# Kernel tuning notes

Hardware: AMD Instinct MI355X
Metric: run time of the kernel (lower is better)

Reference implementation:

```python
import jax, jax.numpy as jnp
import numpy as np

T, B, D, H, A = 512, 256, 256, 256, 8
LOG_STD_MIN, LOG_STD_MAX = -20.0, 2.0


def setup_inputs() -> dict:
    key = jax.random.key(0)
    ks = jax.random.split(key, 5)
    scaled = lambda k, sh, sc: (jax.random.normal(k, sh, jnp.float32) * sc)
    return {
        "x": jax.random.normal(ks[0], (T, B, D), jnp.float32),
        "carry0": jnp.zeros((B, H), jnp.float32),
        # GRU input kernels (ir|iz|in) packed: [D, 3H], shared input bias [3H]
        "Wi": scaled(ks[1], (D, 3 * H), 1.0 / np.sqrt(D)),
        "bi": jnp.zeros((3 * H,), jnp.float32),
        # GRU recurrent kernels (hr|hz|hn) packed: [H, 3H]; only hn has a bias
        "Wh": scaled(ks[2], (H, 3 * H), 1.0 / np.sqrt(H)),
        "bhn": jnp.zeros((H,), jnp.float32),
        # head Dense(2*A) with uniform(0.001)-style small init
        "Wo": scaled(ks[3], (H, 2 * A), 0.001),
        "bo": jnp.zeros((2 * A,), jnp.float32),
    }


def _gru_rollout(x, carry0, Wi, bi, Wh, bhn):
    h_dim = carry0.shape[-1]
    # Precompute input-side gate activations for all timesteps: [T, B, 3H]
    gates_x = x @ Wi + bi

    def step(h, gx):
        gh = h @ Wh  # [B, 3H]
        r = jax.nn.sigmoid(gx[..., :h_dim] + gh[..., :h_dim])
        z = jax.nn.sigmoid(gx[..., h_dim:2 * h_dim] + gh[..., h_dim:2 * h_dim])
        n = jnp.tanh(gx[..., 2 * h_dim:] + r * (gh[..., 2 * h_dim:] + bhn))
        h_new = (1.0 - z) * n + z * h
        return h_new, h_new

    _, carries = jax.lax.scan(step, carry0, gates_x)  # carries: [T, B, H]
    return carries


def reference(x, carry0, Wi, bi, Wh, bhn, Wo, bo):
    carries = _gru_rollout(x, carry0, Wi, bi, Wh, bhn)
    # head -> split into mean / log_std (StdType.MLP_HEAD), clip, exp
    y = carries @ Wo + bo  # [T, B, 2A]
    mean, log_std = jnp.split(y, 2, axis=-1)
    std = jnp.exp(jnp.clip(log_std, LOG_STD_MIN, LOG_STD_MAX))
    # distribution parameters of MultivariateNormalDiag, concatenated
    return jnp.concatenate([mean, std], axis=-1)  # [T, B, 2A]
```

## Files before the change

kernel.cpp:

```cpp
#include <hip/hip_runtime.h>
#include <hip/hip_fp16.h>

typedef _Float16 f16;
typedef __attribute__((ext_vector_type(8))) _Float16 f16x8;
typedef __attribute__((ext_vector_type(4))) _Float16 f16x4;
typedef __attribute__((ext_vector_type(4))) float f32x4;
typedef __attribute__((ext_vector_type(4))) float float4v;
typedef __attribute__((ext_vector_type(4))) int i32x4;

typedef __attribute__((address_space(3))) unsigned int lds_u32;
typedef const __attribute__((address_space(1))) unsigned int glb_u32;


#define CS 0.0039370079f
#define CHEAD 4.805919e-7f
#define FMAGIC 12582912.0f
#define IMAGIC 1262485504

static __device__ __forceinline__ float sigm_s(float x) {
  return __builtin_amdgcn_rcpf(1.0f + __expf(-0.0078125f * x));
}
static __device__ __forceinline__ float tanh_s(float x) {
  float e = __expf(0.015625f * x);
  return 1.0f - 2.0f * __builtin_amdgcn_rcpf(e + 1.0f);
}

__global__ void k_prep_wit(const float* __restrict__ Wi, f16* __restrict__ WiT) {
  __shared__ float tile[32][33];
  const int n0 = blockIdx.x * 32;
  const int k0 = blockIdx.y * 32;
  const int tx = threadIdx.x, ty = threadIdx.y;
#pragma unroll
  for (int i = 0; i < 4; ++i)
    tile[ty + i * 8][tx] = Wi[(size_t)(k0 + ty + i * 8) * 768 + n0 + tx];
  __syncthreads();
#pragma unroll
  for (int i = 0; i < 4; ++i)
    WiT[(size_t)(n0 + ty + i * 8) * 256 + k0 + tx] = (f16)tile[tx][ty + i * 8];
}

__global__ __launch_bounds__(256) void k_x16(const float* __restrict__ x,
                                             f16* __restrict__ x16) {
  size_t i = ((size_t)blockIdx.x * 256 + threadIdx.x) * 4;
  const size_t stride = (size_t)gridDim.x * 1024;
  for (; i < (size_t)512 * 256 * 256; i += stride) {
    float4v v = *reinterpret_cast<const float4v*>(x + i);
    f16x4 h;
    h[0] = (f16)v[0]; h[1] = (f16)v[1]; h[2] = (f16)v[2]; h[3] = (f16)v[3];
    *reinterpret_cast<f16x4*>(x16 + i) = h;
  }
}

__global__ __launch_bounds__(256, 4) void k_gemm_gx16(
    const f16* __restrict__ x16, const f16* __restrict__ WiT,
    const float* __restrict__ bi, f16* __restrict__ gx) {
  __shared__ f16 As[128 * 64];
  __shared__ f16 Bs[128 * 64];
  const int tid = threadIdx.x;
  const int lane = tid & 63;
  const int wave = tid >> 6;
  const int wm = wave >> 1, wn = wave & 1;
  const int m0 = blockIdx.y * 128;
  const int n0 = blockIdx.x * 128;

  const f16* aSrc[4];
  const f16* bSrc[4];
#pragma unroll
  for (int i = 0; i < 4; ++i) {
    const int s = (wave * 4 + i) * 64 + lane;
    const int row = s >> 3, cx = s & 7;
    const int g = cx ^ (row & 7);
    aSrc[i] = x16 + (size_t)(m0 + row) * 256 + g * 8;
    bSrc[i] = WiT + (size_t)(n0 + row) * 256 + g * 8;
  }

  f32x4 acc[4][4] = {};

  for (int ks = 0; ks < 4; ++ks) {
#pragma unroll
    for (int i = 0; i < 4; ++i) {
      __builtin_amdgcn_global_load_lds(
          (glb_u32*)(aSrc[i] + ks * 64),
          (lds_u32*)(reinterpret_cast<char*>(As) + (wave * 4 + i) * 1024), 16, 0, 0);
      __builtin_amdgcn_global_load_lds(
          (glb_u32*)(bSrc[i] + ks * 64),
          (lds_u32*)(reinterpret_cast<char*>(Bs) + (wave * 4 + i) * 1024), 16, 0, 0);
    }
    asm volatile("s_waitcnt vmcnt(0)" ::: "memory");
    __syncthreads();
#pragma unroll
    for (int kt = 0; kt < 2; ++kt) {
      const int kb = kt * 64 + ((lane >> 4) << 4);
      f16x8 a[4], b[4];
#pragma unroll
      for (int mt = 0; mt < 4; ++mt) {
        int r = wm * 64 + mt * 16 + (lane & 15);
        a[mt] = *reinterpret_cast<const f16x8*>(
            reinterpret_cast<const char*>(As) + r * 128 + (kb ^ ((r & 7) << 4)));
      }
#pragma unroll
      for (int nt = 0; nt < 4; ++nt) {
        int r = wn * 64 + nt * 16 + (lane & 15);
        b[nt] = *reinterpret_cast<const f16x8*>(
            reinterpret_cast<const char*>(Bs) + r * 128 + (kb ^ ((r & 7) << 4)));
      }
#pragma unroll
      for (int mt = 0; mt < 4; ++mt)
#pragma unroll
        for (int nt = 0; nt < 4; ++nt)
          acc[mt][nt] = __builtin_amdgcn_mfma_f32_16x16x32_f16(
              a[mt], b[nt], acc[mt][nt], 0, 0, 0);
    }
    __syncthreads();
  }
  const int t_  = blockIdx.y >> 1;
  const int bhf = blockIdx.y & 1;
  const int gg  = blockIdx.x >> 1;
  const int xh  = blockIdx.x & 1;
  float biv[4];
#pragma unroll
  for (int nt = 0; nt < 4; ++nt) biv[nt] = bi[n0 + wn * 64 + nt * 16 + (lane & 15)];
#pragma unroll
  for (int mt = 0; mt < 4; ++mt) {
    const int blk = bhf * 8 + wm * 4 + mt;
#pragma unroll
    for (int nt = 0; nt < 4; ++nt) {
      const int w = xh * 4 + wn * 2 + (nt >> 1);
      const int vecidx = ((t_ * 16 + blk) * 8 + w) * 6 + gg * 2 + (nt & 1);
      f16x4 hv;
#pragma unroll
      for (int r = 0; r < 4; ++r)
        hv[r] = (f16)((acc[mt][nt][r] + biv[nt]) * 128.0f);
      *reinterpret_cast<f16x4*>(gx + (size_t)vecidx * 256 + lane * 4) = hv;
    }
  }
}

__global__ __launch_bounds__(256, 4) void k_gemm_gx(
    const float* __restrict__ x, const f16* __restrict__ WiT,
    const float* __restrict__ bi, f16* __restrict__ gx) {
  __shared__ f16 As[128 * 64];
  __shared__ f16 Bs[128 * 64];
  const int tid = threadIdx.x;
  const int lane = tid & 63;
  const int wave = tid >> 6;
  const int wm = wave >> 1, wn = wave & 1;
  const int m0 = blockIdx.y * 128;
  const int n0 = blockIdx.x * 128;

  f32x4 acc[4][4] = {};

  for (int ks = 0; ks < 4; ++ks) {
    const int k0 = ks * 64;
#pragma unroll
    for (int i = 0; i < 8; ++i) {
      int c = i * 256 + tid;
      int row = c >> 4, cx = c & 15;
      float4v v = *reinterpret_cast<const float4v*>(
          x + (size_t)(m0 + row) * 256 + k0 + cx * 4);
      f16x4 hv;
      hv[0] = (f16)v[0]; hv[1] = (f16)v[1]; hv[2] = (f16)v[2]; hv[3] = (f16)v[3];
      int boff = row * 128 + ((cx * 8) ^ ((row & 7) << 4));
      *reinterpret_cast<f16x4*>(reinterpret_cast<char*>(As) + boff) = hv;
    }
#pragma unroll
    for (int i = 0; i < 4; ++i) {
      int c = i * 256 + tid;
      int n = c >> 3, cx = c & 7;
      f16x8 v = *reinterpret_cast<const f16x8*>(
          WiT + (size_t)(n0 + n) * 256 + k0 + cx * 8);
      int boff = n * 128 + ((cx * 16) ^ ((n & 7) << 4));
      *reinterpret_cast<f16x8*>(reinterpret_cast<char*>(Bs) + boff) = v;
    }
    __syncthreads();
#pragma unroll
    for (int kt = 0; kt < 2; ++kt) {
      const int kb = kt * 64 + ((lane >> 4) << 4);
      f16x8 a[4], b[4];
#pragma unroll
      for (int mt = 0; mt < 4; ++mt) {
        int r = wm * 64 + mt * 16 + (lane & 15);
        a[mt] = *reinterpret_cast<const f16x8*>(
            reinterpret_cast<const char*>(As) + r * 128 + (kb ^ ((r & 7) << 4)));
      }
#pragma unroll
      for (int nt = 0; nt < 4; ++nt) {
        int r = wn * 64 + nt * 16 + (lane & 15);
        b[nt] = *reinterpret_cast<const f16x8*>(
            reinterpret_cast<const char*>(Bs) + r * 128 + (kb ^ ((r & 7) << 4)));
      }
#pragma unroll
      for (int mt = 0; mt < 4; ++mt)
#pragma unroll
        for (int nt = 0; nt < 4; ++nt)
          acc[mt][nt] = __builtin_amdgcn_mfma_f32_16x16x32_f16(
              a[mt], b[nt], acc[mt][nt], 0, 0, 0);
    }
    __syncthreads();
  }
  const int t_  = blockIdx.y >> 1;
  const int bhf = blockIdx.y & 1;
  const int gg  = blockIdx.x >> 1;
  const int xh  = blockIdx.x & 1;
  float biv[4];
#pragma unroll
  for (int nt = 0; nt < 4; ++nt) biv[nt] = bi[n0 + wn * 64 + nt * 16 + (lane & 15)];
#pragma unroll
  for (int mt = 0; mt < 4; ++mt) {
    const int blk = bhf * 8 + wm * 4 + mt;
#pragma unroll
    for (int nt = 0; nt < 4; ++nt) {
      const int w = xh * 4 + wn * 2 + (nt >> 1);
      const int vecidx = ((t_ * 16 + blk) * 8 + w) * 6 + gg * 2 + (nt & 1);
      f16x4 hv;
#pragma unroll
      for (int r = 0; r < 4; ++r)
        hv[r] = (f16)((acc[mt][nt][r] + biv[nt]) * 128.0f);
      *reinterpret_cast<f16x4*>(gx + (size_t)vecidx * 256 + lane * 4) = hv;
    }
  }
}

__global__ __launch_bounds__(1024) void k_scan(
    const float* __restrict__ carry0, const float* __restrict__ Wh,
    const float* __restrict__ bhn, const f16* __restrict__ gxL,
    const float* __restrict__ Wo, const float* __restrict__ bo,
    float* __restrict__ out) {
  __shared__ __align__(16) char ha[8 * 4096];
  __shared__ __align__(16) char wofs[4 * 1024];
  const int tid = threadIdx.x;
  const int lane = tid & 63;
  const int wave = tid >> 6;
  const int l15 = lane & 15, l4 = lane >> 4;
  const int blk = blockIdx.x >> 2;
  const int q = blockIdx.x & 3;
  const int r0 = blk * 16 + q * 4;

  i32x4 whq[3][4];
#pragma unroll
  for (int g = 0; g < 3; ++g) {
    const int col = g * 256 + wave * 16 + l15;
#pragma unroll
    for (int kt = 0; kt < 4; ++kt) {
      int wd[4];
#pragma unroll
      for (int w = 0; w < 4; ++w) {
        int b = 0;
#pragma unroll
        for (int by = 0; by < 4; ++by) {
          const int e = w * 4 + by;
          int qq = (int)rintf(Wh[(size_t)(kt * 64 + l4 * 16 + e) * 768 + col] *
                              256.0f);
          b |= (qq & 255) << (8 * by);
        }
        wd[w] = b;
      }
      whq[g][kt] = (i32x4){wd[0], wd[1], wd[2], wd[3]};
    }
  }
  if (wave < 4) {
    int wd[4];
#pragma unroll
    for (int w = 0; w < 4; ++w) {
      int b = 0;
#pragma unroll
      for (int by = 0; by < 4; ++by) {
        const int e = w * 4 + by;
        int qq = (int)rintf(Wo[(wave * 64 + l4 * 16 + e) * 16 + l15] * 16384.0f);
        b |= (qq & 255) << (8 * by);
      }
      wd[w] = b;
    }
    *reinterpret_cast<i32x4*>(wofs + wave * 1024 + lane * 16) =
        (i32x4){wd[0], wd[1], wd[2], wd[3]};
  }
  const float bh128 = 128.0f * bhn[wave * 16 + l15];
  const float bov = bo[l15];

#pragma unroll
  for (int i = 0; i < 2; ++i)
    *reinterpret_cast<i32x4*>(ha + tid * 32 + i * 16) = (i32x4){0, 0, 0, 0};
  __syncthreads();

  const int wrb = (wave >> 2) * 1024 + ((wave & 3) * 16 + l4 * 4) * 16 + l15;

  float hcur;
  {
    float h = carry0[(size_t)(r0 + l4) * 256 + wave * 16 + l15];
    hcur = h;
    float m = fmaf(h, 127.0f, FMAGIC);
    int hq = __builtin_bit_cast(int, m) - IMAGIC;
    ha[wrb] = (char)hq;
  }
  __syncthreads();

  const f16* gp0 = gxL + (((size_t)blk * 8 + (wave >> 1)) * 6 +
                          (size_t)(wave & 1)) * 256 +
                   (size_t)(q * 16 + l15) * 4 + l4;

  auto head_tau = [&](int tau) {
    const int sbase = (tau & 7) * 4096;
    i32x4 aco = {};
#pragma unroll
    for (int kt = 0; kt < 4; ++kt) {
      i32x4 ah = *reinterpret_cast<const i32x4*>(ha + sbase + kt * 1024 + lane * 16);
      i32x4 wb = *reinterpret_cast<const i32x4*>(wofs + kt * 1024 + lane * 16);
      aco = __builtin_amdgcn_mfma_i32_16x16x64_i8(ah, wb, aco, 0, 0, 0);
    }
    float y = fmaf((float)aco[0], CHEAD, bov);
    if (l15 >= 8) y = __expf(fminf(fmaxf(y, -20.0f), 2.0f));
    out[((size_t)(tau - 1) * 256 + r0 + l4) * 16 + l15] = y;
  };

  f16 gva[3], gvb[3];
#pragma unroll
  for (int g = 0; g < 3; ++g) gva[g] = gp0[g * 512];

  auto step = [&](int cur, int nxt, f16 (&gv)[3], f16 (&gvn)[3],
                  const f16* gpn, int tt) {
    if ((tt & 7) == 0 && tt > 0) {
      if (wave < 8) head_tau(tt - 7 + wave);
      asm volatile("s_waitcnt lgkmcnt(0)\n\ts_barrier" ::: "memory");
    }
#pragma unroll
    for (int g = 0; g < 3; ++g) gvn[g] = gpn[g * 512];

    i32x4 acc0 = {}, acc1 = {}, acc2 = {};
#pragma unroll
    for (int kt = 0; kt < 4; ++kt) {
      i32x4 a = *reinterpret_cast<const i32x4*>(ha + cur + kt * 1024 + lane * 16);
      acc0 = __builtin_amdgcn_mfma_i32_16x16x64_i8(a, whq[0][kt], acc0, 0, 0, 0);
      acc1 = __builtin_amdgcn_mfma_i32_16x16x64_i8(a, whq[1][kt], acc1, 0, 0, 0);
      acc2 = __builtin_amdgcn_mfma_i32_16x16x64_i8(a, whq[2][kt], acc2, 0, 0, 0);
    }

    {
      float pr = fmaf((float)acc0[0], CS, (float)gv[0]);
      float pz = fmaf((float)acc1[0], CS, (float)gv[1]);
      float pnh = fmaf((float)acc2[0], CS, bh128);
      float rg = sigm_s(pr);
      float zg = sigm_s(pz);
      float ng = tanh_s(fmaf(rg, pnh, (float)gv[2]));
      float h = ng + zg * (hcur - ng);
      hcur = h;
      float m = fmaf(h, 127.0f, FMAGIC);
      int hq = __builtin_bit_cast(int, m) - IMAGIC;
      ha[nxt + wrb] = (char)hq;
    }
    asm volatile("s_waitcnt lgkmcnt(0)\n\ts_barrier" ::: "memory");
  };

  for (int t = 0; t < 512; t += 2) {
    const f16* gp1 = gp0 + (size_t)(t + 1) * 196608;
    const f16* gp2 = gp0 + (size_t)(t + 2 <= 511 ? t + 2 : 511) * 196608;
    step((t & 7) * 4096, ((t + 1) & 7) * 4096, gva, gvb, gp1, t);
    step(((t + 1) & 7) * 4096, ((t + 2) & 7) * 4096, gvb, gva, gp2, t + 1);
  }

  if (wave < 8) head_tau(505 + wave);
}

extern "C" void kernel_launch(void* const* d_in, const int* in_sizes, int n_in,
                              void* d_out, int out_size, void* d_ws, size_t ws_size,
                              hipStream_t stream) {
  const float* x      = (const float*)d_in[0];
  const float* carry0 = (const float*)d_in[1];
  const float* Wi     = (const float*)d_in[2];
  const float* bi     = (const float*)d_in[3];
  const float* Wh     = (const float*)d_in[4];
  const float* bhn    = (const float*)d_in[5];
  const float* Wo     = (const float*)d_in[6];
  const float* bo     = (const float*)d_in[7];
  float* out = (float*)d_out;

  f16* gx  = (f16*)d_ws;
  f16* WiT = gx + (size_t)512 * 256 * 768;
  f16* xh  = WiT + (size_t)768 * 256;

  const size_t need = ((size_t)512 * 256 * 768 + (size_t)768 * 256 +
                       (size_t)512 * 256 * 256) * sizeof(f16);

  k_prep_wit<<<dim3(24, 8), dim3(32, 8), 0, stream>>>(Wi, WiT);
  if (ws_size >= need) {
    k_x16<<<dim3(2048), dim3(256), 0, stream>>>(x, xh);
    k_gemm_gx16<<<dim3(6, 1024), dim3(256), 0, stream>>>(xh, WiT, bi, gx);
  } else {
    k_gemm_gx<<<dim3(6, 1024), dim3(256), 0, stream>>>(x, WiT, bi, gx);
  }
  k_scan<<<dim3(64), dim3(1024), 0, stream>>>(carry0, Wh, bhn, gx, Wo, bo, out);
}
```

Measured before the change: 521.9 us.

## Interleave per-step head computation across waves and prioritize MFMA issue

Replaces the batched head computation every 8 steps, which needed its own extra barrier, with one head_tau call per step done by a rotating wave right after the recurrent MFMAs. The A-operand LDS loads are hoisted ahead of the MFMA chain, and s_setprio raises wave priority while the MFMAs issue. This removes one barrier per 8 steps and spreads head work so it overlaps the gate math, at the cost of some per-step imbalance on whichever wave owns the head that step.

```diff
diff --git a/kernel.cpp b/kernel.cpp
--- a/kernel.cpp
+++ b/kernel.cpp
@@ -318,21 +318,31 @@
 
   auto step = [&](int cur, int nxt, f16 (&gv)[3], f16 (&gvn)[3],
                   const f16* gpn, int tt) {
-    if ((tt & 7) == 0 && tt > 0) {
-      if (wave < 8) head_tau(tt - 7 + wave);
-      asm volatile("s_waitcnt lgkmcnt(0)\n\ts_barrier" ::: "memory");
-    }
 #pragma unroll
     for (int g = 0; g < 3; ++g) gvn[g] = gpn[g * 512];
 
+    i32x4 a0 = *reinterpret_cast<const i32x4*>(ha + cur + 0 * 1024 + lane * 16);
+    i32x4 a1 = *reinterpret_cast<const i32x4*>(ha + cur + 1 * 1024 + lane * 16);
+    i32x4 a2 = *reinterpret_cast<const i32x4*>(ha + cur + 2 * 1024 + lane * 16);
+    i32x4 a3 = *reinterpret_cast<const i32x4*>(ha + cur + 3 * 1024 + lane * 16);
+
     i32x4 acc0 = {}, acc1 = {}, acc2 = {};
-#pragma unroll
-    for (int kt = 0; kt < 4; ++kt) {
-      i32x4 a = *reinterpret_cast<const i32x4*>(ha + cur + kt * 1024 + lane * 16);
-      acc0 = __builtin_amdgcn_mfma_i32_16x16x64_i8(a, whq[0][kt], acc0, 0, 0, 0);
-      acc1 = __builtin_amdgcn_mfma_i32_16x16x64_i8(a, whq[1][kt], acc1, 0, 0, 0);
-      acc2 = __builtin_amdgcn_mfma_i32_16x16x64_i8(a, whq[2][kt], acc2, 0, 0, 0);
-    }
+    __builtin_amdgcn_s_setprio(1);
+    acc0 = __builtin_amdgcn_mfma_i32_16x16x64_i8(a0, whq[0][0], acc0, 0, 0, 0);
+    acc1 = __builtin_amdgcn_mfma_i32_16x16x64_i8(a0, whq[1][0], acc1, 0, 0, 0);
+    acc2 = __builtin_amdgcn_mfma_i32_16x16x64_i8(a0, whq[2][0], acc2, 0, 0, 0);
+    acc0 = __builtin_amdgcn_mfma_i32_16x16x64_i8(a1, whq[0][1], acc0, 0, 0, 0);
+    acc1 = __builtin_amdgcn_mfma_i32_16x16x64_i8(a1, whq[1][1], acc1, 0, 0, 0);
+    acc2 = __builtin_amdgcn_mfma_i32_16x16x64_i8(a1, whq[2][1], acc2, 0, 0, 0);
+    acc0 = __builtin_amdgcn_mfma_i32_16x16x64_i8(a2, whq[0][2], acc0, 0, 0, 0);
+    acc1 = __builtin_amdgcn_mfma_i32_16x16x64_i8(a2, whq[1][2], acc1, 0, 0, 0);
+    acc2 = __builtin_amdgcn_mfma_i32_16x16x64_i8(a2, whq[2][2], acc2, 0, 0, 0);
+    acc0 = __builtin_amdgcn_mfma_i32_16x16x64_i8(a3, whq[0][3], acc0, 0, 0, 0);
+    acc1 = __builtin_amdgcn_mfma_i32_16x16x64_i8(a3, whq[1][3], acc1, 0, 0, 0);
+    acc2 = __builtin_amdgcn_mfma_i32_16x16x64_i8(a3, whq[2][3], acc2, 0, 0, 0);
+    __builtin_amdgcn_s_setprio(0);
+
+    if (tt > 0 && wave == (tt & 15)) head_tau(tt);
 
     {
       float pr = fmaf((float)acc0[0], CS, (float)gv[0]);
@@ -357,7 +367,7 @@
     step(((t + 1) & 7) * 4096, ((t + 2) & 7) * 4096, gvb, gva, gp2, t + 1);
   }
 
-  if (wave < 8) head_tau(505 + wave);
+  if (wave == 0) head_tau(512);
 }
 
 extern "C" void kernel_launch(void* const* d_in, const int* in_sizes, int n_in,
```

Result: slower. 620.6 us (+18.9%).
